# Kernel tuning notes

Hardware: AMD Instinct MI355X
Metric: run time of the kernel (lower is better)

## Reference

```python
import math
import jax, jax.numpy as jnp
import numpy as np

D_MODEL = 1024
N_HEAD = 16
HEAD_DIM = D_MODEL // N_HEAD
T = 1.0
EPS = 1e-5  # torch LayerNorm default


def _layernorm(t, gamma, beta):
    # normalize over last dim (head_dim)
    m = t.mean(axis=-1, keepdims=True)
    var = ((t - m) ** 2).mean(axis=-1, keepdims=True)
    return (t - m) * jax.lax.rsqrt(var + EPS) * gamma + beta


def setup_inputs() -> dict:
    key = jax.random.key(0)
    k1, k2, k3 = jax.random.split(key, 3)
    B, S = 4, 2048
    scale = 1.0 / math.sqrt(D_MODEL)
    return {
        "x": jax.random.normal(k1, (B, S, D_MODEL), dtype=jnp.float32),
        "w_qkv": jax.random.normal(k2, (D_MODEL, 3 * D_MODEL), dtype=jnp.float32) * scale,
        "w_proj": jax.random.normal(k3, (D_MODEL, D_MODEL), dtype=jnp.float32) * scale,
        "q_gamma": jnp.ones((HEAD_DIM,), dtype=jnp.float32),
        "q_beta": jnp.zeros((HEAD_DIM,), dtype=jnp.float32),
        "k_gamma": jnp.ones((HEAD_DIM,), dtype=jnp.float32),
        "k_beta": jnp.zeros((HEAD_DIM,), dtype=jnp.float32),
    }


def reference(x, w_qkv, w_proj, q_gamma, q_beta, k_gamma, k_beta):
    B, S, C = x.shape
    H, Dh = N_HEAD, HEAD_DIM
    # QKV projection -> [3, B, H, S, Dh]
    qkv = (x @ w_qkv).reshape(B, S, 3, H, Dh)
    qkv = jnp.transpose(qkv, (2, 0, 3, 1, 4))
    q, k, v = qkv[0], qkv[1], qkv[2]
    # per-head QK LayerNorm
    q = _layernorm(q, q_gamma, q_beta)
    k = _layernorm(k, k_gamma, k_beta)
    # temperature-scaled attention; jax.nn.softmax performs the stable
    # max-subtraction the original does explicitly
    logits = jnp.einsum("bhsd,bhtd->bhst", q, k) / (math.sqrt(Dh) * T)
    att = jax.nn.softmax(logits, axis=-1)
    out = jnp.einsum("bhst,bhtd->bhsd", att, v)
    out = jnp.transpose(out, (0, 2, 1, 3)).reshape(B, S, C)
    return out @ w_proj
```

## Files before the change

kernel.cpp:

```cpp
#include <hip/hip_runtime.h>
#include <stdint.h>

#define D_MODEL 1024
#define NHEAD 16
#define HDIM 64
#define BATCH 4
#define SEQ 2048
#define BS (BATCH*SEQ)
#define NQKV (3*D_MODEL)
#define BHEADS (BATCH*NHEAD)

typedef __bf16 bf16x8 __attribute__((ext_vector_type(8)));
typedef __bf16 bf16x2 __attribute__((ext_vector_type(2)));
typedef float f32x4 __attribute__((ext_vector_type(4)));
typedef float f32x2 __attribute__((ext_vector_type(2)));
typedef float f32x16 __attribute__((ext_vector_type(16)));

__device__ __forceinline__ unsigned short f2bf(float f) {
    union { __bf16 b; unsigned short s; } u; u.b = (__bf16)f; return u.s;
}
__device__ __forceinline__ float bf2f(unsigned short b) {
    union { unsigned u; float f; } v; v.u = ((unsigned)b) << 16;
    return v.f;
}
__device__ __forceinline__ unsigned pack_bf16(float a, float b) {
    f32x2 t; t[0] = a; t[1] = b;
    bf16x2 r = __builtin_convertvector(t, bf16x2);
    union { bf16x2 v; unsigned u; } u; u.v = r; return u.u;
}

typedef __attribute__((address_space(3))) void lds_void_t;
typedef const __attribute__((address_space(1))) void glb_void_t;
__device__ __forceinline__ void gl2lds16(const void* g, void* l) {
    __builtin_amdgcn_global_load_lds((glb_void_t*)g, (lds_void_t*)l, 16, 0, 0);
}

__global__ __launch_bounds__(256) void k_cvt_x(const float4* __restrict__ x,
                                               uint2* __restrict__ o) {
    int i = blockIdx.x * 256 + threadIdx.x;
    float4 v = x[i];
    uint2 r;
    r.x = (unsigned)f2bf(v.x) | ((unsigned)f2bf(v.y) << 16);
    r.y = (unsigned)f2bf(v.z) | ((unsigned)f2bf(v.w) << 16);
    o[i] = r;
}

__global__ __launch_bounds__(256) void k_transpose(const float* __restrict__ in,
                                                   unsigned short* __restrict__ out,
                                                   int ndim) {
    __shared__ float tile[64][65];
    const int n0 = blockIdx.x * 64, k0 = blockIdx.y * 64, tid = threadIdx.x;
#pragma unroll
    for (int i = 0; i < 16; i++) {
        int f = i * 256 + tid; int r = f >> 6, c = f & 63;
        tile[r][c] = in[(size_t)(k0 + r) * ndim + n0 + c];
    }
    __syncthreads();
#pragma unroll
    for (int i = 0; i < 16; i++) {
        int f = i * 256 + tid; int n = f >> 6, kq = f & 63;
        out[(size_t)(n0 + n) * 1024 + k0 + kq] = f2bf(tile[kq][n]);
    }
}

template<int MODE>
__global__ __launch_bounds__(256) void k_gemm(const unsigned short* __restrict__ A,
                                              const unsigned short* __restrict__ Bt,
                                              float* __restrict__ Cout,
                                              unsigned short* __restrict__ qo,
                                              unsigned short* __restrict__ ko,
                                              unsigned short* __restrict__ vto,
                                              const float* __restrict__ qg,
                                              const float* __restrict__ qb,
                                              const float* __restrict__ kg,
                                              const float* __restrict__ kb,
                                              int nbx) {
    __shared__ __align__(16) unsigned short smem[16384];
    unsigned short* As = smem;
    unsigned short* Bs = smem + 8192;
    const int tid = threadIdx.x, lane = tid & 63, wid = tid >> 6;
    const int l16 = lane & 15, lq = lane >> 4;
    const int wr = wid >> 1, wc = wid & 1;

    const int nwg = nbx * gridDim.y;
    int bid = blockIdx.x + nbx * blockIdx.y;
    int swz = (bid & 7) * (nwg >> 3) + (bid >> 3);
    const int bx = swz % nbx, by = swz / nbx;
    const int M0 = bx * 128, N0 = by * 128;

    f32x4 acc[4][4] = {};

    for (int k0 = 0; k0 < 1024; k0 += 64) {
#pragma unroll
        for (int i = 0; i < 4; i++) {
            int g = i * 256 + tid;
            int r = g >> 3, c = (g & 7) * 8;
            int ldsbase = (i * 256 + wid * 64) * 8;
            gl2lds16(A  + (size_t)(M0 + r) * 1024 + k0 + c, &As[ldsbase]);
            gl2lds16(Bt + (size_t)(N0 + r) * 1024 + k0 + c, &Bs[ldsbase]);
        }
        __syncthreads();
#pragma unroll
        for (int kk = 0; kk < 2; kk++) {
            bf16x8 af[4], bfr[4];
#pragma unroll
            for (int m = 0; m < 4; m++)
                af[m] = *(const bf16x8*)&As[(wr * 64 + m * 16 + l16) * 64 + kk * 32 + lq * 8];
#pragma unroll
            for (int n = 0; n < 4; n++)
                bfr[n] = *(const bf16x8*)&Bs[(wc * 64 + n * 16 + l16) * 64 + kk * 32 + lq * 8];
#pragma unroll
            for (int m = 0; m < 4; m++)
#pragma unroll
                for (int n = 0; n < 4; n++)
                    acc[m][n] = __builtin_amdgcn_mfma_f32_16x16x32_bf16(af[m], bfr[n], acc[m][n], 0, 0, 0);
        }
        __syncthreads();
    }

    if (MODE == 1) {
#pragma unroll
        for (int m = 0; m < 4; m++)
#pragma unroll
            for (int n = 0; n < 4; n++)
#pragma unroll
                for (int r = 0; r < 4; r++) {
                    int row = M0 + wr * 64 + m * 16 + lq * 4 + r;
                    int col = N0 + wc * 64 + n * 16 + l16;
                    Cout[(size_t)row * 1024 + col] = acc[m][n][r];
                }
        return;
    }

    const int colbase = N0 + wc * 64;
    const int which = colbase >> 10;
    const int h = (colbase >> 6) & 15;
    const int b = M0 >> 11;
    const int bh = (b << 4) + h;
    const int srow0 = (M0 & 2047) + wr * 64;

    if (which == 2) {
        unsigned short* tw = smem + wid * 4096;
#pragma unroll
        for (int m = 0; m < 4; m++)
#pragma unroll
            for (int n = 0; n < 4; n++)
#pragma unroll
                for (int r = 0; r < 4; r++) {
                    int s_l = m * 16 + lq * 4 + r;
                    int d = n * 16 + l16;
                    tw[d * 64 + (s_l ^ ((d & 7) << 3))] = f2bf(acc[m][n][r]);
                }
        asm volatile("" ::: "memory");
        unsigned short* vtb = vto + (size_t)bh * 64 * SEQ + srow0;
#pragma unroll
        for (int j = 0; j < 8; j++) {
            int d_r = j * 8 + (lane >> 3);
            int s8 = (lane & 7) * 8;
            bf16x8 val = *(const bf16x8*)&tw[d_r * 64 + (s8 ^ ((d_r & 7) << 3))];
            *(bf16x8*)(vtb + (size_t)d_r * SEQ + s8) = val;
        }
        return;
    }

    unsigned short* outp = which ? ko : qo;
    const float* gp = which ? kg : qg;
    const float* bp = which ? kb : qb;
    const float cs = which ? 1.0f : 0.18033688011112042f;
    float gv[4], bv[4];
#pragma unroll
    for (int n = 0; n < 4; n++) { gv[n] = gp[n * 16 + l16]; bv[n] = bp[n * 16 + l16]; }

#pragma unroll
    for (int m = 0; m < 4; m++) {
        f32x4 s1 = acc[m][0] + acc[m][1] + acc[m][2] + acc[m][3];
        f32x4 s2 = acc[m][0] * acc[m][0] + acc[m][1] * acc[m][1]
                 + acc[m][2] * acc[m][2] + acc[m][3] * acc[m][3];
#pragma unroll
        for (int mask = 1; mask < 16; mask <<= 1) {
#pragma unroll
            for (int r = 0; r < 4; r++) {
                s1[r] += __shfl_xor(s1[r], mask);
                s2[r] += __shfl_xor(s2[r], mask);
            }
        }
        f32x4 mean = s1 * 0.015625f;
        f32x4 rstd;
#pragma unroll
        for (int r = 0; r < 4; r++) {
            float var = s2[r] * 0.015625f - mean[r] * mean[r];
            rstd[r] = rsqrtf(var + 1e-5f);
        }
#pragma unroll
        for (int n = 0; n < 4; n++) {
            int d = n * 16 + l16;
#pragma unroll
            for (int r = 0; r < 4; r++) {
                int s = srow0 + m * 16 + lq * 4 + r;
                float val = ((acc[m][n][r] - mean[r]) * rstd[r] * gv[n] + bv[n]) * cs;
                outp[((size_t)bh * SEQ + s) * 64 + d] = f2bf(val);
            }
        }
    }
}

__global__ __launch_bounds__(256, 4) void k_flash(const unsigned short* __restrict__ q,
                                                  const unsigned short* __restrict__ k,
                                                  const unsigned short* __restrict__ vt,
                                                  unsigned short* __restrict__ aout) {
    __shared__ __align__(16) unsigned short Ks[2][64 * 64];
    __shared__ __align__(16) unsigned short Vs[2][64 * 64];
    const int tid = threadIdx.x, lane = tid & 63, wid = tid >> 6;
    const int l32 = lane & 31, hi = lane >> 5;
    const int bh = blockIdx.x;
    const int q0 = blockIdx.y * 128 + wid * 32;

    const unsigned short* qrow = q + ((size_t)bh * SEQ + q0 + l32) * 64 + hi * 8;
    bf16x8 bq[4];
#pragma unroll
    for (int t = 0; t < 4; t++)
        bq[t] = *(const bf16x8*)(qrow + t * 16);

    const unsigned short* kp[2];
    const unsigned short* vp[2];
#pragma unroll
    for (int i = 0; i < 2; i++) {
        int s = i * 256 + tid;
        int row = s >> 3, gsrc = (s & 7) ^ (row & 7);
        kp[i] = k  + (size_t)bh * SEQ * 64 + (size_t)row * 64  + gsrc * 8;
        vp[i] = vt + (size_t)bh * 64 * SEQ + (size_t)row * SEQ + gsrc * 8;
    }
#pragma unroll
    for (int i = 0; i < 2; i++) {
        int ldsoff = (i * 256 + wid * 64) * 8;
        gl2lds16(kp[i], &Ks[0][ldsoff]);
        gl2lds16(vp[i], &Vs[0][ldsoff]);
        kp[i] += 64 * 64; vp[i] += 64;
    }
    __syncthreads();

    f32x16 o0 = {}, o1 = {};
    float l_run = 0.f;
    const int xs = (l32 & 7);

    f32x16 minit;
#pragma unroll
    for (int r = 0; r < 16; r++) minit[r] = -12.0f;

    for (int t = 0; t < SEQ / 64; t++) {
        const int cur = t & 1;
        if (t + 1 < SEQ / 64) {
#pragma unroll
            for (int i = 0; i < 2; i++) {
                int ldsoff = (i * 256 + wid * 64) * 8;
                gl2lds16(kp[i], &Ks[cur ^ 1][ldsoff]);
                gl2lds16(vp[i], &Vs[cur ^ 1][ldsoff]);
                kp[i] += 64 * 64; vp[i] += 64;
            }
        }

        f32x16 sa0 = minit, sa1 = minit;
        __builtin_amdgcn_s_setprio(1);
#pragma unroll
        for (int ks = 0; ks < 4; ks++) {
            int gx = (((ks * 2 + hi) ^ xs) * 8);
            bf16x8 ak0 = *(const bf16x8*)&Ks[cur][l32 * 64 + gx];
            bf16x8 ak1 = *(const bf16x8*)&Ks[cur][(32 + l32) * 64 + gx];
            sa0 = __builtin_amdgcn_mfma_f32_32x32x16_bf16(ak0, bq[ks], sa0, 0, 0, 0);
            sa1 = __builtin_amdgcn_mfma_f32_32x32x16_bf16(ak1, bq[ks], sa1, 0, 0, 0);
        }
        __builtin_amdgcn_s_setprio(0);

        f32x16 p0, p1;
#pragma unroll
        for (int r = 0; r < 16; r++) p0[r] = __builtin_amdgcn_exp2f(sa0[r]);
#pragma unroll
        for (int r = 0; r < 16; r++) p1[r] = __builtin_amdgcn_exp2f(sa1[r]);

        f32x16 ts = p0 + p1;
        f32x4 s4;
#pragma unroll
        for (int j = 0; j < 4; j++)
            s4[j] = (ts[j] + ts[j + 4]) + (ts[j + 8] + ts[j + 12]);
        float rs = (s4[0] + s4[1]) + (s4[2] + s4[3]);
        rs += __shfl_xor(rs, 32);
        l_run += rs;

        union BP { unsigned w[4]; bf16x8 v; };
        BP bpf[4];
#pragma unroll
        for (int ks = 0; ks < 4; ks++) {
            const f32x16& ps = (ks >> 1) ? p1 : p0;
            const int base = (ks & 1) * 8;
            unsigned a0 = pack_bf16(ps[base + 0], ps[base + 1]);
            unsigned a1 = pack_bf16(ps[base + 2], ps[base + 3]);
            unsigned b0 = pack_bf16(ps[base + 4], ps[base + 5]);
            unsigned b1 = pack_bf16(ps[base + 6], ps[base + 7]);
            asm volatile("v_permlane32_swap_b32 %0, %1" : "+v"(a0), "+v"(b0));
            asm volatile("v_permlane32_swap_b32 %0, %1" : "+v"(a1), "+v"(b1));
            bpf[ks].w[0] = a0; bpf[ks].w[1] = a1; bpf[ks].w[2] = b0; bpf[ks].w[3] = b1;
        }

        __builtin_amdgcn_s_setprio(1);
#pragma unroll
        for (int ks = 0; ks < 4; ks++) {
            int gx = (((ks * 2 + hi) ^ xs) * 8);
            bf16x8 av0 = *(const bf16x8*)&Vs[cur][l32 * 64 + gx];
            bf16x8 av1 = *(const bf16x8*)&Vs[cur][(32 + l32) * 64 + gx];
            o0 = __builtin_amdgcn_mfma_f32_32x32x16_bf16(av0, bpf[ks].v, o0, 0, 0, 0);
            o1 = __builtin_amdgcn_mfma_f32_32x32x16_bf16(av1, bpf[ks].v, o1, 0, 0, 0);
        }
        __builtin_amdgcn_s_setprio(0);
        __syncthreads();
    }

    float inv = 1.0f / l_run;
    const int b = bh >> 4, h = bh & 15;
    unsigned short* orow = aout + ((size_t)b * SEQ + q0 + l32) * 1024 + h * 64;
#pragma unroll
    for (int dblk = 0; dblk < 2; dblk++) {
        const f32x16& oo = dblk ? o1 : o0;
#pragma unroll
        for (int q2 = 0; q2 < 4; q2++) {
            ushort4 u4;
            u4.x = f2bf(oo[q2 * 4 + 0] * inv);
            u4.y = f2bf(oo[q2 * 4 + 1] * inv);
            u4.z = f2bf(oo[q2 * 4 + 2] * inv);
            u4.w = f2bf(oo[q2 * 4 + 3] * inv);
            *(ushort4*)(orow + dblk * 32 + q2 * 8 + hi * 4) = u4;
        }
    }
}

extern "C" void kernel_launch(void* const* d_in, const int* in_sizes, int n_in,
                              void* d_out, int out_size, void* d_ws, size_t ws_size,
                              hipStream_t stream) {
    const float* x     = (const float*)d_in[0];
    const float* wqkv  = (const float*)d_in[1];
    const float* wproj = (const float*)d_in[2];
    const float* qg    = (const float*)d_in[3];
    const float* qb    = (const float*)d_in[4];
    const float* kg    = (const float*)d_in[5];
    const float* kb    = (const float*)d_in[6];
    float* out = (float*)d_out;

    char* ws = (char*)d_ws;
    unsigned short* xbf    = (unsigned short*)(ws);
    unsigned short* wqkvT  = (unsigned short*)(ws + (16llu << 20));
    unsigned short* wprojT = (unsigned short*)(ws + (22llu << 20));
    unsigned short* qraw   = (unsigned short*)(ws + (24llu << 20));
    unsigned short* kraw   = (unsigned short*)(ws + (40llu << 20));
    unsigned short* vtr    = (unsigned short*)(ws + (56llu << 20));
    unsigned short* aattn  = (unsigned short*)(ws + (72llu << 20));

    hipLaunchKernelGGL(k_cvt_x, dim3(8192), dim3(256), 0, stream, (const float4*)x, (uint2*)xbf);
    hipLaunchKernelGGL(k_transpose, dim3(48, 16), dim3(256), 0, stream, wqkv, wqkvT, 3072);
    hipLaunchKernelGGL(k_transpose, dim3(16, 16), dim3(256), 0, stream, wproj, wprojT, 1024);
    hipLaunchKernelGGL((k_gemm<0>), dim3(64, 24), dim3(256), 0, stream, xbf, wqkvT, (float*)nullptr,
                       qraw, kraw, vtr, qg, qb, kg, kb, 64);
    hipLaunchKernelGGL(k_flash, dim3(64, 16), dim3(256), 0, stream, qraw, kraw, vtr, aattn);
    hipLaunchKernelGGL((k_gemm<1>), dim3(64, 8), dim3(256), 0, stream, aattn, wprojT, out,
                       (unsigned short*)nullptr, (unsigned short*)nullptr, (unsigned short*)nullptr,
                       (const float*)nullptr, (const float*)nullptr, (const float*)nullptr,
                       (const float*)nullptr, 64);
}
```

Baseline: 221.9 us.

## Swap MFMA operands for Q/K tiles to vectorize LayerNorm epilogue and stores

For the Q and K column tiles of the QKV GEMM, the MFMA operands are swapped so each lane holds four consecutive head-dim values of one row instead of four rows. The per-row LayerNorm reduction then needs only two cross-lane shuffles instead of eight per statistic, and outputs go out as 8-byte vector stores rather than scattered 2-byte stores. The block-index swizzle is also changed to a different XCD-aware tile mapping. The cost is a templated duplicate of the K loop, which adds code size and a branch on the tile type.

```diff
diff --git a/kernel.cpp b/kernel.cpp
--- a/kernel.cpp
+++ b/kernel.cpp
@@ -15,6 +15,9 @@
 typedef float f32x4 __attribute__((ext_vector_type(4)));
 typedef float f32x2 __attribute__((ext_vector_type(2)));
 typedef float f32x16 __attribute__((ext_vector_type(16)));
+
+struct TrueT  { static constexpr bool value = true;  };
+struct FalseT { static constexpr bool value = false; };
 
 __device__ __forceinline__ unsigned short f2bf(float f) {
     union { __bf16 b; unsigned short s; } u; u.b = (__bf16)f; return u.s;
@@ -82,41 +85,55 @@
     const int l16 = lane & 15, lq = lane >> 4;
     const int wr = wid >> 1, wc = wid & 1;
 
-    const int nwg = nbx * gridDim.y;
-    int bid = blockIdx.x + nbx * blockIdx.y;
-    int swz = (bid & 7) * (nwg >> 3) + (bid >> 3);
-    const int bx = swz % nbx, by = swz / nbx;
+    const int ny = gridDim.y;
+    const int bid = blockIdx.x + nbx * blockIdx.y;
+    const int xcd = bid & 7, idx = bid >> 3;
+    const int by = idx % ny;
+    const int bx = xcd * (nbx >> 3) + idx / ny;
     const int M0 = bx * 128, N0 = by * 128;
 
+    const int colbase = N0 + wc * 64;
+    const int which = (MODE == 0) ? (colbase >> 10) : 3;
+
     f32x4 acc[4][4] = {};
 
-    for (int k0 = 0; k0 < 1024; k0 += 64) {
-#pragma unroll
-        for (int i = 0; i < 4; i++) {
-            int g = i * 256 + tid;
-            int r = g >> 3, c = (g & 7) * 8;
-            int ldsbase = (i * 256 + wid * 64) * 8;
-            gl2lds16(A  + (size_t)(M0 + r) * 1024 + k0 + c, &As[ldsbase]);
-            gl2lds16(Bt + (size_t)(N0 + r) * 1024 + k0 + c, &Bs[ldsbase]);
-        }
-        __syncthreads();
-#pragma unroll
-        for (int kk = 0; kk < 2; kk++) {
-            bf16x8 af[4], bfr[4];
-#pragma unroll
-            for (int m = 0; m < 4; m++)
-                af[m] = *(const bf16x8*)&As[(wr * 64 + m * 16 + l16) * 64 + kk * 32 + lq * 8];
-#pragma unroll
-            for (int n = 0; n < 4; n++)
-                bfr[n] = *(const bf16x8*)&Bs[(wc * 64 + n * 16 + l16) * 64 + kk * 32 + lq * 8];
-#pragma unroll
-            for (int m = 0; m < 4; m++)
+    auto kloop = [&](auto SWAPC) {
+        constexpr bool SWAP = decltype(SWAPC)::value;
+        for (int k0 = 0; k0 < 1024; k0 += 64) {
+#pragma unroll
+            for (int i = 0; i < 4; i++) {
+                int g = i * 256 + tid;
+                int r = g >> 3, c = (g & 7) * 8;
+                int ldsbase = (i * 256 + wid * 64) * 8;
+                gl2lds16(A  + (size_t)(M0 + r) * 1024 + k0 + c, &As[ldsbase]);
+                gl2lds16(Bt + (size_t)(N0 + r) * 1024 + k0 + c, &Bs[ldsbase]);
+            }
+            __syncthreads();
+#pragma unroll
+            for (int kk = 0; kk < 2; kk++) {
+                bf16x8 af[4], bfr[4];
+#pragma unroll
+                for (int m = 0; m < 4; m++)
+                    af[m] = *(const bf16x8*)&As[(wr * 64 + m * 16 + l16) * 64 + kk * 32 + lq * 8];
 #pragma unroll
                 for (int n = 0; n < 4; n++)
-                    acc[m][n] = __builtin_amdgcn_mfma_f32_16x16x32_bf16(af[m], bfr[n], acc[m][n], 0, 0, 0);
-        }
-        __syncthreads();
-    }
+                    bfr[n] = *(const bf16x8*)&Bs[(wc * 64 + n * 16 + l16) * 64 + kk * 32 + lq * 8];
+#pragma unroll
+                for (int m = 0; m < 4; m++)
+#pragma unroll
+                    for (int n = 0; n < 4; n++) {
+                        if constexpr (SWAP)
+                            acc[m][n] = __builtin_amdgcn_mfma_f32_16x16x32_bf16(bfr[n], af[m], acc[m][n], 0, 0, 0);
+                        else
+                            acc[m][n] = __builtin_amdgcn_mfma_f32_16x16x32_bf16(af[m], bfr[n], acc[m][n], 0, 0, 0);
+                    }
+            }
+            __syncthreads();
+        }
+    };
+
+    const bool swapped = (MODE == 0) && (which < 2);
+    if (swapped) kloop(TrueT{}); else kloop(FalseT{});
 
     if (MODE == 1) {
 #pragma unroll
@@ -132,8 +149,6 @@
         return;
     }
 
-    const int colbase = N0 + wc * 64;
-    const int which = colbase >> 10;
     const int h = (colbase >> 6) & 15;
     const int b = M0 >> 11;
     const int bh = (b << 4) + h;
@@ -167,39 +182,34 @@
     const float* gp = which ? kg : qg;
     const float* bp = which ? kb : qb;
     const float cs = which ? 1.0f : 0.18033688011112042f;
-    float gv[4], bv[4];
-#pragma unroll
-    for (int n = 0; n < 4; n++) { gv[n] = gp[n * 16 + l16]; bv[n] = bp[n * 16 + l16]; }
+    f32x4 gv[4], bv4[4];
+#pragma unroll
+    for (int n = 0; n < 4; n++) {
+        gv[n]  = *(const f32x4*)(gp + n * 16 + lq * 4);
+        bv4[n] = *(const f32x4*)(bp + n * 16 + lq * 4);
+    }
 
 #pragma unroll
     for (int m = 0; m < 4; m++) {
-        f32x4 s1 = acc[m][0] + acc[m][1] + acc[m][2] + acc[m][3];
-        f32x4 s2 = acc[m][0] * acc[m][0] + acc[m][1] * acc[m][1]
+        f32x4 t1 = acc[m][0] + acc[m][1] + acc[m][2] + acc[m][3];
+        f32x4 t2 = acc[m][0] * acc[m][0] + acc[m][1] * acc[m][1]
                  + acc[m][2] * acc[m][2] + acc[m][3] * acc[m][3];
-#pragma unroll
-        for (int mask = 1; mask < 16; mask <<= 1) {
-#pragma unroll
-            for (int r = 0; r < 4; r++) {
-                s1[r] += __shfl_xor(s1[r], mask);
-                s2[r] += __shfl_xor(s2[r], mask);
-            }
-        }
-        f32x4 mean = s1 * 0.015625f;
-        f32x4 rstd;
-#pragma unroll
-        for (int r = 0; r < 4; r++) {
-            float var = s2[r] * 0.015625f - mean[r] * mean[r];
-            rstd[r] = rsqrtf(var + 1e-5f);
-        }
+        float s1 = (t1[0] + t1[1]) + (t1[2] + t1[3]);
+        float s2 = (t2[0] + t2[1]) + (t2[2] + t2[3]);
+        s1 += __shfl_xor(s1, 16);  s1 += __shfl_xor(s1, 32);
+        s2 += __shfl_xor(s2, 16);  s2 += __shfl_xor(s2, 32);
+        float mean = s1 * 0.015625f;
+        float rstd = rsqrtf(s2 * 0.015625f - mean * mean + 1e-5f);
+        int s = srow0 + m * 16 + l16;
+        unsigned short* rowp = outp + ((size_t)bh * SEQ + s) * 64;
 #pragma unroll
         for (int n = 0; n < 4; n++) {
-            int d = n * 16 + l16;
-#pragma unroll
-            for (int r = 0; r < 4; r++) {
-                int s = srow0 + m * 16 + lq * 4 + r;
-                float val = ((acc[m][n][r] - mean[r]) * rstd[r] * gv[n] + bv[n]) * cs;
-                outp[((size_t)bh * SEQ + s) * 64 + d] = f2bf(val);
-            }
+            ushort4 u4;
+            u4.x = f2bf(((acc[m][n][0] - mean) * rstd * gv[n][0] + bv4[n][0]) * cs);
+            u4.y = f2bf(((acc[m][n][1] - mean) * rstd * gv[n][1] + bv4[n][1]) * cs);
+            u4.z = f2bf(((acc[m][n][2] - mean) * rstd * gv[n][2] + bv4[n][2]) * cs);
+            u4.w = f2bf(((acc[m][n][3] - mean) * rstd * gv[n][3] + bv4[n][3]) * cs);
+            *(ushort4*)(rowp + n * 16 + lq * 4) = u4;
         }
     }
 }
```

Result: faster. 214.3 us (-3.4%).
